# Kernel optimization log

Measured on AMD Instinct MI355X. Metric: run time of the kernel, lower is better.

The kernel has to match this reference:

```python
import jax, jax.numpy as jnp
import numpy as np

RPN_CLS_NEGATIVE = -1
RPN_CLS_NEUTRAL = 0
RPN_CLS_POSITIVE = 1

A = 261888  # anchors for 1024x1024 FPN, 3 per location
G = 256     # gt boxes


def _make_boxes(key, n, max_tl=900.0, min_sz=16.0, max_sz=124.0):
    k1, k2 = jax.random.split(key)
    tl = jax.random.uniform(k1, (n, 2), dtype=jnp.float32) * max_tl  # (y1, x1)
    wh = min_sz + jax.random.uniform(k2, (n, 2), dtype=jnp.float32) * (max_sz - min_sz)
    return jnp.concatenate([tl, tl + wh], axis=1)  # (y1, x1, y2, x2), all coords > 0


def setup_inputs() -> dict:
    key = jax.random.key(0)
    ka, kg, km, kc = jax.random.split(key, 4)
    anchors = _make_boxes(ka, A)
    gt_boxes = _make_boxes(kg, G)
    valid_anchors_mask = jax.random.uniform(km, (A,)) > 0.1
    gt_class_ids = jax.random.randint(kc, (G,), 1, 81, dtype=jnp.int32)
    bbox_std_dev = jnp.array([0.1, 0.1, 0.2, 0.2], dtype=jnp.float32)
    return {
        "anchors": anchors,
        "valid_anchors_mask": valid_anchors_mask,
        "gt_class_ids": gt_class_ids,
        "gt_boxes": gt_boxes,
        "bbox_std_dev": bbox_std_dev,
    }


def _compute_overlaps(b1, b2):
    """Pairwise IoU. b1: [N,4], b2: [M,4] -> [N,M]."""
    y1 = jnp.maximum(b1[:, None, 0], b2[None, :, 0])
    x1 = jnp.maximum(b1[:, None, 1], b2[None, :, 1])
    y2 = jnp.minimum(b1[:, None, 2], b2[None, :, 2])
    x2 = jnp.minimum(b1[:, None, 3], b2[None, :, 3])
    inter = jnp.maximum(y2 - y1, 0.0) * jnp.maximum(x2 - x1, 0.0)
    area1 = (b1[:, 2] - b1[:, 0]) * (b1[:, 3] - b1[:, 1])
    area2 = (b2[:, 2] - b2[:, 0]) * (b2[:, 3] - b2[:, 1])
    union = area1[:, None] + area2[None, :] - inter
    return inter / union


def reference(anchors, valid_anchors_mask, gt_class_ids, gt_boxes, bbox_std_dev):
    num_anchors = anchors.shape[0]
    is_crowd = gt_class_ids < 0  # [G]
    any_crowd = jnp.any(is_crowd)

    overlaps = _compute_overlaps(anchors, gt_boxes)  # [A, G]

    # crowd suppression (vectorized equivalent of the numpy crowd branch)
    crowd_iou_max = jnp.max(jnp.where(is_crowd[None, :], overlaps, 0.0), axis=1)
    no_crowd = jnp.where(any_crowd, crowd_iou_max < 0.001, True)

    # mask crowd columns out of the matching (numpy filters them from gt_boxes)
    ov = jnp.where(is_crowd[None, :], -1.0, overlaps)  # [A, G]
    anchor_iou_argmax = jnp.argmax(ov, axis=1)          # [A]
    anchor_iou_max = jnp.max(ov, axis=1)                # [A]

    # per-GT best anchor, restricted to valid anchors (numpy works on valid subset)
    ov_valid = jnp.where(valid_anchors_mask[:, None], ov, -1.0)
    gt_iou_argmax = jnp.argmax(ov_valid, axis=0)        # [G]
    pos_from_gt = jnp.zeros((num_anchors,), dtype=bool).at[gt_iou_argmax].max(~is_crowd)

    positive = pos_from_gt | (anchor_iou_max >= 0.7)
    negative = (anchor_iou_max < 0.3) & no_crowd & (~positive)

    rpn_match = jnp.where(positive, RPN_CLS_POSITIVE,
                          jnp.where(negative, RPN_CLS_NEGATIVE, RPN_CLS_NEUTRAL)).astype(jnp.int32)
    rpn_match = jnp.where(valid_anchors_mask, rpn_match, RPN_CLS_NEUTRAL)

    # deltas for positive anchors (faithful to source, incl. the `- -` -> `+` size bug)
    matched_gt = gt_boxes[anchor_iou_argmax]            # [A, 4]
    gt_size = matched_gt[:, 2:4] + matched_gt[:, 0:2]   # source: b[:,2:4] - -b[:,0:2]
    gt_centre = (matched_gt[:, 0:2] + matched_gt[:, 2:4]) * 0.5
    anc_size = anchors[:, 2:4] + anchors[:, 0:2]        # same bug
    anc_centre = (anchors[:, 0:2] + anchors[:, 2:4]) * 0.5
    deltas = jnp.concatenate([(gt_centre - anc_centre) / anc_size,
                              jnp.log(gt_size / anc_size)], axis=1)  # [A, 4]
    deltas = deltas / bbox_std_dev[None, :]  # RPN_BBOX_USE_STD_DEV = True

    pos_valid = positive & valid_anchors_mask
    rpn_bbox_all = jnp.where(pos_valid[:, None], deltas, 0.0).astype(jnp.float32)
    num_positives = jnp.sum(pos_valid).astype(jnp.int32)
    return rpn_match, rpn_bbox_all, num_positives
```

## Files before the change

kernel.cpp:

```cpp
#include <hip/hip_runtime.h>


#define GMAX 256
#define SHARDS 64
#define KBIAS 0xC0000001u
#define AIMASK 0x3FFFFu

__device__ __forceinline__ float4 compute_deltas(float4 ab, float4 gb,
                                                 const float* __restrict__ sd) {
    float sy_g = gb.z + gb.x;
    float sx_g = gb.w + gb.y;
    float sy_a = ab.z + ab.x;
    float sx_a = ab.w + ab.y;
    float4 d;
    d.x = (0.5f * (sy_g - sy_a) / sy_a) / sd[0];
    d.y = (0.5f * (sx_g - sx_a) / sx_a) / sd[1];
    d.z = logf(sy_g / sy_a) / sd[2];
    d.w = logf(sx_g / sx_a) / sd[3];
    return d;
}

__device__ __forceinline__ float iou_from(float4 ab, float a_area, float4 gb,
                                          float ga, float& inter) {
#pragma clang fp contract(off)
    float y1 = fmaxf(ab.x, gb.x);
    float x1 = fmaxf(ab.y, gb.y);
    float y2 = fminf(ab.z, gb.z);
    float x2 = fminf(ab.w, gb.w);
    inter = fmaxf(y2 - y1, 0.f) * fmaxf(x2 - x1, 0.f);
    return inter * __builtin_amdgcn_rcpf((a_area + ga) - inter);
}

__device__ __forceinline__ float iou_of(float4 ab, float a_area, float4 gb) {
    float y1 = fmaxf(ab.x, gb.x);
    float x1 = fmaxf(ab.y, gb.y);
    float y2 = fminf(ab.z, gb.z);
    float x2 = fminf(ab.w, gb.w);
    float inter = fmaxf(y2 - y1, 0.f) * fmaxf(x2 - x1, 0.f);
    float garea = (gb.z - gb.x) * (gb.w - gb.y);
    float uni = (a_area + garea) - inter;
    return inter * __builtin_amdgcn_rcpf(uni);
}

__global__ __launch_bounds__(256, 8) void rpn_main6(
    const float4* __restrict__ anchors,
    const int* __restrict__ valid,
    const int* __restrict__ cls,
    const float4* __restrict__ gt,
    const float* __restrict__ stdev,
    float* __restrict__ out,
    unsigned long long* __restrict__ gkeyS,
    int* __restrict__ pcount,
    int* __restrict__ fvmin,
    int A, int G)
{
    __shared__ float4 s_gt[GMAX];
    __shared__ float s_area[GMAX];
    __shared__ float s_crowdf[GMAX];
    __shared__ unsigned long long s_key[GMAX];
    __shared__ int s_anycrowd;
    __shared__ int s_cnt;
    __shared__ int s_fv;

    const int tid = threadIdx.x;
    if (tid == 0) { s_anycrowd = 0; s_cnt = 0; s_fv = 0x7FFFFFFF; }
    s_key[tid] = 0ULL;
    if (tid < G) {
        float4 b = gt[tid];
        s_gt[tid] = b;
        s_area[tid] = (b.z - b.x) * (b.w - b.y);
        int c = cls[tid];
        s_crowdf[tid] = (c < 0) ? 1.0f : 0.0f;
        if (c < 0) s_anycrowd = 1;
    }
    __syncthreads();
    const int any_crowd = s_anycrowd;

    const int a  = tid >> 2;
    const int h  = tid & 3;
    const int ai = blockIdx.x * 64 + a;
    const bool ir = (ai < A);
    float4 ab = ir ? anchors[ai] : make_float4(0.f, 0.f, 1.f, 1.f);
    const bool v = ir && (valid[ai] != 0);
    const float a_area = (ab.z - ab.x) * (ab.w - ab.y);

    const bool fast = (!any_crowd && G == GMAX);
    const int Gq = (G + 3) >> 2;

    float best = 0.0f;
    float cm = 0.0f;
    unsigned long long mm = 0ULL;
    int bg_final = 0;

    if (fast) {
        const float4* gp  = &s_gt[h];
        const float*  apb = &s_area[h];
        #pragma unroll
        for (int j = 0; j < 64; ++j) {
            float it;
            float iou = iou_from(ab, a_area, gp[j << 2], apb[j << 2], it);
            best = fmaxf(best, iou);
            if (it > 0.0f) mm |= (1ULL << j);
        }

        best = fmaxf(best, __shfl_xor(best, 1));
        best = fmaxf(best, __shfl_xor(best, 2));

        int bg_eq = 0x7FFFFFFF;
        if (best > 0.0f) {
            unsigned long long m = mm;
            while (m != 0ULL) {
                int j = __builtin_ctzll(m); m &= (m - 1ULL);
                int g = (j << 2) + h;
                float it;
                float iou = iou_from(ab, a_area, s_gt[g], s_area[g], it);
                if (iou == best) { bg_eq = g; break; }
            }
        }
        bg_eq = min(bg_eq, __shfl_xor(bg_eq, 1));
        bg_eq = min(bg_eq, __shfl_xor(bg_eq, 2));
        if (bg_eq != 0x7FFFFFFF) bg_final = bg_eq;
    } else {
        const int g0 = h * Gq;
        const int gn = max(0, min(G - g0, Gq));
        float bestg = -2.0f;
        int bg = min(g0, G - 1);
        for (int gg = 0; gg < gn; ++gg) {
            const int g = g0 + gg;
            float it;
            float iou = iou_from(ab, a_area, s_gt[g], s_area[g], it);
            float cf = s_crowdf[g];
            float eff = (cf != 0.0f) ? -1.0f : iou;
            if (eff > bestg) { bestg = eff; bg = g; }
            cm = fmaxf(cm, iou * cf);
            if (cf == 0.0f && iou > 0.0f) mm |= (1ULL << gg);
        }
        #pragma unroll
        for (int off = 1; off <= 2; off <<= 1) {
            float ob  = __shfl_xor(bestg, off);
            int   obg = __shfl_xor(bg, off);
            float ocm = __shfl_xor(cm, off);
            if (ob > bestg || (ob == bestg && obg < bg)) { bestg = ob; bg = obg; }
            cm = fmaxf(cm, ocm);
        }
        best = bestg;
        bg_final = bg;
    }

    bool no_crowd = any_crowd ? (cm < 0.001f) : true;
    bool pos = (best >= 0.7f);
    bool neg = (best < 0.3f) && no_crowd && !pos;
    bool posv = (h == 0) && pos && v;

    if (ir && h == 0) {
        out[ai] = v ? (pos ? 1.0f : (neg ? -1.0f : 0.0f)) : 0.0f;
        float4 d = make_float4(0.f, 0.f, 0.f, 0.f);
        if (pos && v) d = compute_deltas(ab, s_gt[bg_final], stdev);
        ((float4*)(out + A))[ai] = d;
    }

    if (v) {
        if (h == 0) atomicMin(&s_fv, ai);
        const unsigned long long lo =
            (((unsigned long long)((~(unsigned)ai) & AIMASK)) << 8) |
            (unsigned long long)((unsigned)bg_final & 0xFFu);
        unsigned long long m = mm;
        while (m != 0ULL) {
            int j = __builtin_ctzll(m); m &= (m - 1ULL);
            const int g = fast ? ((j << 2) + h) : (h * Gq + j);
            float it;
            float iou = iou_from(ab, a_area, s_gt[g], s_area[g], it);
            atomicMax(&s_key[g],
                (((unsigned long long)(__float_as_uint(iou) + KBIAS)) << 32) | lo);
        }
    }

    unsigned long long bal = __ballot((int)posv);
    if ((tid & 63) == 0) atomicAdd(&s_cnt, (int)__popcll(bal));
    __syncthreads();

    if (tid < G && s_key[tid] != 0ULL)
        atomicMax(&gkeyS[(size_t)tid * SHARDS + (blockIdx.x & (SHARDS - 1))],
                  s_key[tid]);
    if (tid == 0) { pcount[blockIdx.x] = s_cnt; fvmin[blockIdx.x] = s_fv; }
}

__global__ __launch_bounds__(1024) void rpn_finalize3(
    const float4* __restrict__ anchors,
    const int* __restrict__ cls,
    const float4* __restrict__ gt,
    const float* __restrict__ stdev,
    float* __restrict__ out,
    const unsigned long long* __restrict__ gkeyS,
    const int* __restrict__ pcount,
    const int* __restrict__ fvmin,
    int nb, int A, int G)
{
    __shared__ float4 s_gt[GMAX];
    __shared__ float s_area[GMAX];
    __shared__ float s_crowdf[GMAX];
    __shared__ int s_tot, s_fvr, s_flip;

    const int tid = threadIdx.x;
    if (tid == 0) { s_tot = 0; s_fvr = 0x7FFFFFFF; s_flip = 0; }
    if (tid < G) {
        float4 b = gt[tid];
        s_gt[tid] = b;
        s_area[tid] = (b.z - b.x) * (b.w - b.y);
        s_crowdf[tid] = (cls[tid] < 0) ? 1.0f : 0.0f;
    }
    __syncthreads();

    unsigned long long key = 0ULL;
    if (tid < G) {
        const unsigned long long* p = gkeyS + (size_t)tid * SHARDS;
        #pragma unroll
        for (int s = 0; s < SHARDS; s += 2) {
            ulonglong2 kv = *reinterpret_cast<const ulonglong2*>(p + s);
            unsigned long long k = (kv.x > kv.y) ? kv.x : kv.y;
            key = (k > key) ? k : key;
        }
    }
    if (tid >= 256) {
        int acc = 0, fv = 0x7FFFFFFF;
        for (int i = tid - 256; i < nb; i += 768) {
            acc += pcount[i];
            fv = min(fv, fvmin[i]);
        }
        #pragma unroll
        for (int off = 32; off >= 1; off >>= 1) {
            acc += __shfl_xor(acc, off);
            fv = min(fv, __shfl_xor(fv, off));
        }
        if ((tid & 63) == 0) { atomicAdd(&s_tot, acc); atomicMin(&s_fvr, fv); }
    }
    __syncthreads();

    bool flipped = false;
    if (tid < G && s_crowdf[tid] == 0.0f) {
        const bool has = ((unsigned)(key >> 32) >= (KBIAS + 1u));
        int w = -1, bg = -1;
        if (has) {
            w  = (int)((~((unsigned)key >> 8)) & AIMASK);
            bg = (int)((unsigned)key & 0xFFu);
        } else if (s_fvr != 0x7FFFFFFF) {
            w = s_fvr;
        }
        if (w >= 0) {
            float old = atomicExch(out + w, 1.0f);
            if (old != 1.0f) {
                if (bg < 0) {
                    float4 ab = anchors[w];
                    float aa = (ab.z - ab.x) * (ab.w - ab.y);
                    float bb = -2.0f; bg = 0;
                    for (int g = 0; g < G; ++g) {
                        float it;
                        float iou = iou_from(ab, aa, s_gt[g], s_area[g], it);
                        float eff = (s_crowdf[g] != 0.0f) ? -1.0f : iou;
                        if (eff > bb) { bb = eff; bg = g; }
                    }
                }
                ((float4*)(out + A))[w] = compute_deltas(anchors[w], s_gt[bg], stdev);
                flipped = true;
            }
        }
    }
    unsigned long long fb = __ballot((int)flipped);
    if (tid < 256 && (tid & 63) == 0) atomicAdd(&s_flip, (int)__popcll(fb));
    __syncthreads();
    if (tid == 0) out[(size_t)5 * A] = (float)(s_tot + s_flip);
}

__global__ __launch_bounds__(256) void rpn_fused(
    const float4* __restrict__ anchors, const int* __restrict__ valid,
    const int* __restrict__ cls, const float4* __restrict__ gt,
    const float* __restrict__ stdev, float* __restrict__ out,
    unsigned long long* __restrict__ gkey, unsigned* __restrict__ done,
    int* __restrict__ cnt, int A, int G)
{
    __shared__ float4 s_gt[GMAX];
    __shared__ float s_crowdf[GMAX];
    __shared__ unsigned long long s_key[GMAX];
    __shared__ int s_anycrowd; __shared__ int s_cnt; __shared__ int s_islast;

    const int tid = threadIdx.x;
    if (tid == 0) { s_anycrowd = 0; s_cnt = 0; }
    if (tid < G) {
        s_gt[tid] = gt[tid];
        int c = cls[tid];
        s_crowdf[tid] = (c < 0) ? 1.0f : 0.0f;
        if (c < 0) s_anycrowd = 1;
        s_key[tid] = 0ULL;
    }
    __syncthreads();
    const int any_crowd = s_anycrowd;
    const int ai = blockIdx.x * 256 + tid;
    const bool in_range = (ai < A);
    float4 ab = in_range ? anchors[ai] : make_float4(0.f, 0.f, 1.f, 1.f);
    const bool v = in_range && (valid[ai] != 0);
    const float a_area = (ab.z - ab.x) * (ab.w - ab.y);
    const unsigned lokey = ~(unsigned)ai;

    float best = any_crowd ? -2.0f : -1.0f;
    int bg = 0; float crowd_max = 0.0f;
    unsigned long long ovmask[4];
    #pragma unroll
    for (int w = 0; w < 4; ++w) {
        unsigned long long m = 0ULL;
        #pragma unroll 4
        for (int j = 0; j < 64; ++j) {
            int g = (w << 6) + j;
            if (g >= G) break;
            float iou = iou_of(ab, a_area, s_gt[g]);
            float cf = s_crowdf[g];
            float eff = (any_crowd && cf != 0.0f) ? -1.0f : iou;
            if (eff > best) { best = eff; bg = g; }
            if (any_crowd) crowd_max = fmaxf(crowd_max, iou * cf);
            if (v && (cf == 0.0f) && iou > 0.0f) m |= (1ULL << j);
        }
        ovmask[w] = m;
    }
    #pragma unroll
    for (int w = 0; w < 4; ++w) {
        unsigned long long m = ovmask[w];
        while (m != 0ULL) {
            int j = __builtin_ctzll(m); m &= (m - 1ULL);
            int g = (w << 6) + j;
            float iou = iou_of(ab, a_area, s_gt[g]);
            atomicMax(&s_key[g],
                (((unsigned long long)(__float_as_uint(iou) + 1u)) << 32) | lokey);
        }
    }
    bool no_crowd = any_crowd ? (crowd_max < 0.001f) : true;
    bool pos = (best >= 0.7f);
    bool neg = (best < 0.3f) && no_crowd && !pos;
    unsigned long long pv = __ballot((int)(in_range && pos && v));
    if ((tid & 63) == 0) atomicAdd(&s_cnt, (int)__popcll(pv));
    if (in_range) {
        out[ai] = v ? (pos ? 1.0f : (neg ? -1.0f : 0.0f)) : 0.0f;
        float4 d = make_float4(0.f, 0.f, 0.f, 0.f);
        if (pos && v) d = compute_deltas(ab, s_gt[bg], stdev);
        ((float4*)(out + A))[ai] = d;
    }
    __syncthreads();
    if (tid < G && s_key[tid] != 0ULL) atomicMax(&gkey[tid], s_key[tid]);
    if (tid == 0 && s_cnt > 0) atomicAdd(cnt, s_cnt);
    __threadfence();
    if (tid == 0) {
        unsigned prev = atomicAdd(done, 1u);
        s_islast = (prev == gridDim.x - 1);
        s_cnt = 0;
    }
    __syncthreads();
    if (!s_islast) return;
    __threadfence();
    if (tid < G && s_crowdf[tid] == 0.0f) {
        unsigned long long key = gkey[tid];
        int w;
        if (key != 0ULL) w = (int)(~(unsigned)(key & 0xFFFFFFFFull));
        else { w = 0; for (int i = 0; i < A; ++i) { if (valid[i] != 0) { w = i; break; } } }
        if (valid[w] != 0) {
            float old = atomicExch(out + w, 1.0f);
            if (old != 1.0f) {
                float4 ab2 = anchors[w];
                float a2 = (ab2.z - ab2.x) * (ab2.w - ab2.y);
                float b2 = -2.0f; int g2 = 0;
                for (int g = 0; g < G; ++g) {
                    float iou = iou_of(ab2, a2, s_gt[g]);
                    float eff = (s_crowdf[g] != 0.0f) ? -1.0f : iou;
                    if (eff > b2) { b2 = eff; g2 = g; }
                }
                ((float4*)(out + A))[w] = compute_deltas(ab2, s_gt[g2], stdev);
                atomicAdd(&s_cnt, 1);
            }
        }
    }
    __syncthreads();
    if (tid == 0) out[(size_t)5 * A] = (float)(*cnt + s_cnt);
}

extern "C" void kernel_launch(void* const* d_in, const int* in_sizes, int n_in,
                              void* d_out, int out_size, void* d_ws, size_t ws_size,
                              hipStream_t stream) {
    const float4* anchors = (const float4*)d_in[0];
    const int* valid      = (const int*)d_in[1];
    const int* cls        = (const int*)d_in[2];
    const float4* gtb     = (const float4*)d_in[3];
    const float* stdev    = (const float*)d_in[4];
    float* out            = (float*)d_out;

    const int A = in_sizes[0] / 4;
    const int G = in_sizes[2];
    const int nb4 = (A + 63) / 64;

    const size_t shard_bytes = (size_t)G * SHARDS * 8;
    const size_t pcnt_bytes  = (size_t)nb4 * 4;
    const size_t fv_bytes    = (size_t)nb4 * 4;
    const size_t needed = shard_bytes + pcnt_bytes + fv_bytes;

    if (ws_size >= needed && G <= GMAX && A <= (1 << 18)) {
        char* p = (char*)d_ws;
        unsigned long long* gkeyS = (unsigned long long*)p;          p += shard_bytes;
        int* pcount               = (int*)p;                         p += pcnt_bytes;
        int* fvmin                = (int*)p;

        rpn_main6<<<nb4, 256, 0, stream>>>(anchors, valid, cls, gtb, stdev, out,
                                           gkeyS, pcount, fvmin, A, G);
        rpn_finalize3<<<1, 1024, 0, stream>>>(anchors, cls, gtb, stdev, out,
                                              gkeyS, pcount, fvmin, nb4, A, G);
    } else {
        const int nb = (A + 255) / 256;
        unsigned long long* gkey = (unsigned long long*)d_ws;
        unsigned* done = (unsigned*)((char*)d_ws + 2048);
        int* cnt       = (int*)((char*)d_ws + 2052);
        hipMemsetAsync(d_ws, 0, 2056, stream);
        rpn_fused<<<nb, 256, 0, stream>>>(anchors, valid, cls, gtb, stdev, out,
                                          gkey, done, cnt, A, G);
    }
}
```

Baseline: 119.2 us.

## Bin gt boxes into a spatial grid per block to prune IoU candidates

Each block now buckets the gt boxes into an 8x8 grid of 128-pixel cells by their top-left corner, using a shared-memory prefix sum, and finds the largest gt height and width. Each anchor then computes IoU only against gt boxes in cells that could overlap it, instead of all 256, for both the best-match search and the per-gt max-key atomics. This cuts per-anchor IoU work, at the cost of extra setup and barriers in every block, data-dependent loop trip counts that cause divergence, and relying on gt coordinates being non-negative for correct binning.

```diff
diff --git a/kernel.cpp b/kernel.cpp
--- a/kernel.cpp
+++ b/kernel.cpp
@@ -42,7 +42,7 @@
     return inter * __builtin_amdgcn_rcpf(uni);
 }
 
-__global__ __launch_bounds__(256, 8) void rpn_main6(
+__global__ __launch_bounds__(256, 8) void rpn_main7(
     const float4* __restrict__ anchors,
     const int* __restrict__ valid,
     const int* __restrict__ cls,
@@ -58,13 +58,21 @@
     __shared__ float s_area[GMAX];
     __shared__ float s_crowdf[GMAX];
     __shared__ unsigned long long s_key[GMAX];
-    __shared__ int s_anycrowd;
-    __shared__ int s_cnt;
-    __shared__ int s_fv;
+    __shared__ unsigned short s_cellgt[GMAX];
+    __shared__ int s_cell[64];
+    __shared__ int s_cellcnt[64];
+    __shared__ int s_cur[64];
+    __shared__ int s_mhi, s_mwi;
+    __shared__ int s_anycrowd, s_cnt, s_fv;
 
     const int tid = threadIdx.x;
-    if (tid == 0) { s_anycrowd = 0; s_cnt = 0; s_fv = 0x7FFFFFFF; }
+    const float inv = 0.0078125f;
+    if (tid == 0) { s_anycrowd = 0; s_cnt = 0; s_fv = 0x7FFFFFFF; s_mhi = 0; s_mwi = 0; }
+    if (tid < 64) s_cellcnt[tid] = 0;
     s_key[tid] = 0ULL;
+
+    float gh = 0.f, gw = 0.f;
+    int mycell = 0;
     if (tid < G) {
         float4 b = gt[tid];
         s_gt[tid] = b;
@@ -72,9 +80,45 @@
         int c = cls[tid];
         s_crowdf[tid] = (c < 0) ? 1.0f : 0.0f;
         if (c < 0) s_anycrowd = 1;
-    }
-    __syncthreads();
+        gh = fmaxf(b.z - b.x, 0.f);
+        gw = fmaxf(b.w - b.y, 0.f);
+        int rr = max(0, min(7, (int)(b.x * inv)));
+        int cc = max(0, min(7, (int)(b.y * inv)));
+        mycell = (rr << 3) + cc;
+    }
+    #pragma unroll
+    for (int off = 32; off >= 1; off >>= 1) {
+        gh = fmaxf(gh, __shfl_xor(gh, off));
+        gw = fmaxf(gw, __shfl_xor(gw, off));
+    }
+    __syncthreads();
+    if (tid < G) atomicAdd(&s_cellcnt[mycell], 1);
+    if ((tid & 63) == 0) {
+        atomicMax(&s_mhi, __float_as_int(gh));
+        atomicMax(&s_mwi, __float_as_int(gw));
+    }
+    __syncthreads();
+    if (tid < 64) {
+        int v0 = s_cellcnt[tid];
+        int incl = v0;
+        #pragma unroll
+        for (int off = 1; off < 64; off <<= 1) {
+            int n = __shfl_up(incl, off);
+            if (tid >= off) incl += n;
+        }
+        s_cell[tid] = (incl - v0) | (v0 << 16);
+        s_cur[tid]  = incl - v0;
+    }
+    __syncthreads();
+    if (tid < G) {
+        int slot = atomicAdd(&s_cur[mycell], 1);
+        s_cellgt[slot] = (unsigned short)tid;
+    }
+    __syncthreads();
+
     const int any_crowd = s_anycrowd;
+    const float mh = __int_as_float(s_mhi);
+    const float mw = __int_as_float(s_mwi);
 
     const int a  = tid >> 2;
     const int h  = tid & 3;
@@ -84,45 +128,67 @@
     const bool v = ir && (valid[ai] != 0);
     const float a_area = (ab.z - ab.x) * (ab.w - ab.y);
 
-    const bool fast = (!any_crowd && G == GMAX);
-    const int Gq = (G + 3) >> 2;
-
     float best = 0.0f;
     float cm = 0.0f;
-    unsigned long long mm = 0ULL;
     int bg_final = 0;
 
-    if (fast) {
-        const float4* gp  = &s_gt[h];
-        const float*  apb = &s_area[h];
+    if (any_crowd == 0) {
+        float t0 = (ab.x - mh) * inv;
+        const int r0 = (t0 <= 0.f) ? 0 : min(7, (int)t0);
+        const int r1 = min(7, max(0, (int)(ab.z * inv)));
+        float u0 = (ab.y - mw) * inv;
+        const int c0 = (u0 <= 0.f) ? 0 : min(7, (int)u0);
+        const int c1 = min(7, max(0, (int)(ab.w * inv)));
+
+        float bb = 0.f; int bg = 0;
+        for (int r = r0; r <= r1; ++r) {
+            for (int c = c0; c <= c1; ++c) {
+                const unsigned sc = (unsigned)s_cell[(r << 3) + c];
+                const int start = (int)(sc & 0xFFFFu);
+                const int cnt   = (int)(sc >> 16);
+                for (int k = h; k < cnt; k += 4) {
+                    const int g = (int)s_cellgt[start + k];
+                    float it;
+                    float iou = iou_from(ab, a_area, s_gt[g], s_area[g], it);
+                    if (iou > bb) { bb = iou; bg = g; }
+                    else if (iou == bb && g < bg) bg = g;
+                }
+            }
+        }
         #pragma unroll
-        for (int j = 0; j < 64; ++j) {
-            float it;
-            float iou = iou_from(ab, a_area, gp[j << 2], apb[j << 2], it);
-            best = fmaxf(best, iou);
-            if (it > 0.0f) mm |= (1ULL << j);
-        }
-
-        best = fmaxf(best, __shfl_xor(best, 1));
-        best = fmaxf(best, __shfl_xor(best, 2));
-
-        int bg_eq = 0x7FFFFFFF;
-        if (best > 0.0f) {
-            unsigned long long m = mm;
-            while (m != 0ULL) {
-                int j = __builtin_ctzll(m); m &= (m - 1ULL);
-                int g = (j << 2) + h;
-                float it;
-                float iou = iou_from(ab, a_area, s_gt[g], s_area[g], it);
-                if (iou == best) { bg_eq = g; break; }
+        for (int off = 1; off <= 2; off <<= 1) {
+            float ob = __shfl_xor(bb, off);
+            int  obg = __shfl_xor(bg, off);
+            if (ob > bb || (ob == bb && obg < bg)) { bb = ob; bg = obg; }
+        }
+        best = bb; bg_final = bg;
+
+        if (v) {
+            if (h == 0) atomicMin(&s_fv, ai);
+            const unsigned long long lo =
+                (((unsigned long long)((~(unsigned)ai) & AIMASK)) << 8) |
+                (unsigned long long)((unsigned)bg_final & 0xFFu);
+            for (int r = r0; r <= r1; ++r) {
+                for (int c = c0; c <= c1; ++c) {
+                    const unsigned sc = (unsigned)s_cell[(r << 3) + c];
+                    const int start = (int)(sc & 0xFFFFu);
+                    const int cnt   = (int)(sc >> 16);
+                    for (int k = h; k < cnt; k += 4) {
+                        const int g = (int)s_cellgt[start + k];
+                        float it;
+                        float iou = iou_from(ab, a_area, s_gt[g], s_area[g], it);
+                        if (it > 0.f)
+                            atomicMax(&s_key[g],
+                                (((unsigned long long)(__float_as_uint(iou) + KBIAS)) << 32) | lo);
+                    }
+                }
             }
         }
-        bg_eq = min(bg_eq, __shfl_xor(bg_eq, 1));
-        bg_eq = min(bg_eq, __shfl_xor(bg_eq, 2));
-        if (bg_eq != 0x7FFFFFFF) bg_final = bg_eq;
     } else {
+        const int Gq = (G + 3) >> 2;
         const int g0 = h * Gq;
         const int gn = max(0, min(G - g0, Gq));
+        unsigned long long mm = 0ULL;
         float bestg = -2.0f;
         int bg = min(g0, G - 1);
         for (int gg = 0; gg < gn; ++gg) {
@@ -143,8 +209,23 @@
             if (ob > bestg || (ob == bestg && obg < bg)) { bestg = ob; bg = obg; }
             cm = fmaxf(cm, ocm);
         }
-        best = bestg;
-        bg_final = bg;
+        best = bestg; bg_final = bg;
+
+        if (v) {
+            if (h == 0) atomicMin(&s_fv, ai);
+            const unsigned long long lo =
+                (((unsigned long long)((~(unsigned)ai) & AIMASK)) << 8) |
+                (unsigned long long)((unsigned)bg_final & 0xFFu);
+            unsigned long long m = mm;
+            while (m != 0ULL) {
+                int j = __builtin_ctzll(m); m &= (m - 1ULL);
+                const int g = g0 + j;
+                float it;
+                float iou = iou_from(ab, a_area, s_gt[g], s_area[g], it);
+                atomicMax(&s_key[g],
+                    (((unsigned long long)(__float_as_uint(iou) + KBIAS)) << 32) | lo);
+            }
+        }
     }
 
     bool no_crowd = any_crowd ? (cm < 0.001f) : true;
@@ -157,22 +238,6 @@
         float4 d = make_float4(0.f, 0.f, 0.f, 0.f);
         if (pos && v) d = compute_deltas(ab, s_gt[bg_final], stdev);
         ((float4*)(out + A))[ai] = d;
-    }
-
-    if (v) {
-        if (h == 0) atomicMin(&s_fv, ai);
-        const unsigned long long lo =
-            (((unsigned long long)((~(unsigned)ai) & AIMASK)) << 8) |
-            (unsigned long long)((unsigned)bg_final & 0xFFu);
-        unsigned long long m = mm;
-        while (m != 0ULL) {
-            int j = __builtin_ctzll(m); m &= (m - 1ULL);
-            const int g = fast ? ((j << 2) + h) : (h * Gq + j);
-            float it;
-            float iou = iou_from(ab, a_area, s_gt[g], s_area[g], it);
-            atomicMax(&s_key[g],
-                (((unsigned long long)(__float_as_uint(iou) + KBIAS)) << 32) | lo);
-        }
     }
 
     unsigned long long bal = __ballot((int)posv);
@@ -404,7 +469,7 @@
         int* pcount               = (int*)p;                         p += pcnt_bytes;
         int* fvmin                = (int*)p;
 
-        rpn_main6<<<nb4, 256, 0, stream>>>(anchors, valid, cls, gtb, stdev, out,
+        rpn_main7<<<nb4, 256, 0, stream>>>(anchors, valid, cls, gtb, stdev, out,
                                            gkeyS, pcount, fvmin, A, G);
         rpn_finalize3<<<1, 1024, 0, stream>>>(anchors, cls, gtb, stdev, out,
                                               gkeyS, pcount, fvmin, nb4, A, G);
```

New measurement: 123.7 us. 3.8% more time.

## Process four anchors per thread to reuse each GT load across anchors

Applied to the files above, without the earlier changes.

Each block now covers 256 anchors instead of 64. In the fast path every thread evaluates four anchors against its quarter of the GT boxes, so each shared-memory GT load is reused four times. Per-thread results are picked out with select helpers for the output writes, and the first-valid-anchor tracking moves to a ballot-based atomicMin. The slow crowd path becomes one anchor per thread scanning all GTs. The cost is higher register pressure (launch bounds relaxed to 4 blocks) and four times fewer blocks, which feeds into the finalize kernel's per-block arrays.

```diff
diff --git a/kernel.cpp b/kernel.cpp
--- a/kernel.cpp
+++ b/kernel.cpp
@@ -42,7 +42,26 @@
     return inter * __builtin_amdgcn_rcpf(uni);
 }
 
-__global__ __launch_bounds__(256, 8) void rpn_main6(
+__device__ __forceinline__ float sel4f(float a0, float a1, float a2, float a3, int h) {
+    float lo = (h & 1) ? a1 : a0;
+    float hi = (h & 1) ? a3 : a2;
+    return (h & 2) ? hi : lo;
+}
+__device__ __forceinline__ int sel4i(int a0, int a1, int a2, int a3, int h) {
+    int lo = (h & 1) ? a1 : a0;
+    int hi = (h & 1) ? a3 : a2;
+    return (h & 2) ? hi : lo;
+}
+__device__ __forceinline__ float4 sel4f4(float4 a0, float4 a1, float4 a2, float4 a3, int h) {
+    float4 r;
+    r.x = sel4f(a0.x, a1.x, a2.x, a3.x, h);
+    r.y = sel4f(a0.y, a1.y, a2.y, a3.y, h);
+    r.z = sel4f(a0.z, a1.z, a2.z, a3.z, h);
+    r.w = sel4f(a0.w, a1.w, a2.w, a3.w, h);
+    return r;
+}
+
+__global__ __launch_bounds__(256, 4) void rpn_main8(
     const float4* __restrict__ anchors,
     const int* __restrict__ valid,
     const int* __restrict__ cls,
@@ -58,9 +77,7 @@
     __shared__ float s_area[GMAX];
     __shared__ float s_crowdf[GMAX];
     __shared__ unsigned long long s_key[GMAX];
-    __shared__ int s_anycrowd;
-    __shared__ int s_cnt;
-    __shared__ int s_fv;
+    __shared__ int s_anycrowd, s_cnt, s_fv;
 
     const int tid = threadIdx.x;
     if (tid == 0) { s_anycrowd = 0; s_cnt = 0; s_fv = 0x7FFFFFFF; }
@@ -76,107 +93,158 @@
     __syncthreads();
     const int any_crowd = s_anycrowd;
 
-    const int a  = tid >> 2;
-    const int h  = tid & 3;
-    const int ai = blockIdx.x * 64 + a;
-    const bool ir = (ai < A);
-    float4 ab = ir ? anchors[ai] : make_float4(0.f, 0.f, 1.f, 1.f);
-    const bool v = ir && (valid[ai] != 0);
-    const float a_area = (ab.z - ab.x) * (ab.w - ab.y);
-
-    const bool fast = (!any_crowd && G == GMAX);
-    const int Gq = (G + 3) >> 2;
-
-    float best = 0.0f;
-    float cm = 0.0f;
-    unsigned long long mm = 0ULL;
-    int bg_final = 0;
-
-    if (fast) {
+    const int q = tid >> 2;
+    const int h = tid & 3;
+    const int abase = blockIdx.x * 256 + (q << 2);
+    const int myai  = blockIdx.x * 256 + tid;
+    const bool myir = (myai < A);
+
+    bool posv = false, vmy = false;
+
+    if (!any_crowd && G == GMAX) {
+        float4 ab[4]; float aar[4]; int vld[4];
+        #pragma unroll
+        for (int k = 0; k < 4; ++k) {
+            const int ak = abase + k;
+            const bool irk = (ak < A);
+            ab[k]  = irk ? anchors[ak] : make_float4(0.f, 0.f, 1.f, 1.f);
+            vld[k] = irk ? valid[ak] : 0;
+            aar[k] = (ab[k].z - ab[k].x) * (ab[k].w - ab[k].y);
+        }
+
+        float best[4] = {0.f, 0.f, 0.f, 0.f};
+        unsigned long long msk[4] = {0ULL, 0ULL, 0ULL, 0ULL};
         const float4* gp  = &s_gt[h];
         const float*  apb = &s_area[h];
-        #pragma unroll
+        #pragma unroll 8
         for (int j = 0; j < 64; ++j) {
-            float it;
-            float iou = iou_from(ab, a_area, gp[j << 2], apb[j << 2], it);
-            best = fmaxf(best, iou);
-            if (it > 0.0f) mm |= (1ULL << j);
-        }
-
-        best = fmaxf(best, __shfl_xor(best, 1));
-        best = fmaxf(best, __shfl_xor(best, 2));
-
-        int bg_eq = 0x7FFFFFFF;
-        if (best > 0.0f) {
-            unsigned long long m = mm;
-            while (m != 0ULL) {
-                int j = __builtin_ctzll(m); m &= (m - 1ULL);
-                int g = (j << 2) + h;
+            float4 gb = gp[j << 2];
+            float  ga = apb[j << 2];
+            #pragma unroll
+            for (int k = 0; k < 4; ++k) {
                 float it;
-                float iou = iou_from(ab, a_area, s_gt[g], s_area[g], it);
-                if (iou == best) { bg_eq = g; break; }
-            }
-        }
-        bg_eq = min(bg_eq, __shfl_xor(bg_eq, 1));
-        bg_eq = min(bg_eq, __shfl_xor(bg_eq, 2));
-        if (bg_eq != 0x7FFFFFFF) bg_final = bg_eq;
+                float iou = iou_from(ab[k], aar[k], gb, ga, it);
+                best[k] = fmaxf(best[k], iou);
+                if (it > 0.f) msk[k] |= (1ULL << j);
+            }
+        }
+
+        float mb[4];
+        #pragma unroll
+        for (int k = 0; k < 4; ++k) {
+            float b = best[k];
+            b = fmaxf(b, __shfl_xor(b, 1));
+            b = fmaxf(b, __shfl_xor(b, 2));
+            mb[k] = b;
+        }
+        int bgm[4];
+        #pragma unroll
+        for (int k = 0; k < 4; ++k) {
+            int be = 0x7FFFFFFF;
+            if (mb[k] > 0.f) {
+                unsigned long long m = msk[k];
+                while (m != 0ULL) {
+                    int j = __builtin_ctzll(m); m &= (m - 1ULL);
+                    int g = (j << 2) + h;
+                    float it;
+                    float iou = iou_from(ab[k], aar[k], s_gt[g], s_area[g], it);
+                    if (iou == mb[k]) { be = g; break; }
+                }
+            }
+            be = min(be, __shfl_xor(be, 1));
+            be = min(be, __shfl_xor(be, 2));
+            bgm[k] = (be == 0x7FFFFFFF) ? 0 : be;
+        }
+
+        const float4 abm = sel4f4(ab[0], ab[1], ab[2], ab[3], h);
+        const float  mbm = sel4f(mb[0], mb[1], mb[2], mb[3], h);
+        const int    bgmy = sel4i(bgm[0], bgm[1], bgm[2], bgm[3], h);
+        const int    vm   = sel4i(vld[0], vld[1], vld[2], vld[3], h);
+        vmy = myir && (vm != 0);
+        bool pos = (mbm >= 0.7f);
+        bool neg = (mbm < 0.3f) && !pos;
+        posv = pos && vmy;
+        if (myir) {
+            out[myai] = vmy ? (pos ? 1.0f : (neg ? -1.0f : 0.0f)) : 0.0f;
+            float4 d = make_float4(0.f, 0.f, 0.f, 0.f);
+            if (pos && vmy) d = compute_deltas(abm, s_gt[bgmy], stdev);
+            ((float4*)(out + A))[myai] = d;
+        }
+
+        #pragma unroll
+        for (int k = 0; k < 4; ++k) {
+            if (vld[k]) {
+                const unsigned long long lo =
+                    (((unsigned long long)((~(unsigned)(abase + k)) & AIMASK)) << 8) |
+                    (unsigned long long)((unsigned)bgm[k] & 0xFFu);
+                unsigned long long m = msk[k];
+                while (m != 0ULL) {
+                    int j = __builtin_ctzll(m); m &= (m - 1ULL);
+                    int g = (j << 2) + h;
+                    float it;
+                    float iou = iou_from(ab[k], aar[k], s_gt[g], s_area[g], it);
+                    atomicMax(&s_key[g],
+                        (((unsigned long long)(__float_as_uint(iou) + KBIAS)) << 32) | lo);
+                }
+            }
+        }
     } else {
-        const int g0 = h * Gq;
-        const int gn = max(0, min(G - g0, Gq));
-        float bestg = -2.0f;
-        int bg = min(g0, G - 1);
-        for (int gg = 0; gg < gn; ++gg) {
-            const int g = g0 + gg;
-            float it;
-            float iou = iou_from(ab, a_area, s_gt[g], s_area[g], it);
-            float cf = s_crowdf[g];
-            float eff = (cf != 0.0f) ? -1.0f : iou;
-            if (eff > bestg) { bestg = eff; bg = g; }
-            cm = fmaxf(cm, iou * cf);
-            if (cf == 0.0f && iou > 0.0f) mm |= (1ULL << gg);
-        }
-        #pragma unroll
-        for (int off = 1; off <= 2; off <<= 1) {
-            float ob  = __shfl_xor(bestg, off);
-            int   obg = __shfl_xor(bg, off);
-            float ocm = __shfl_xor(cm, off);
-            if (ob > bestg || (ob == bestg && obg < bg)) { bestg = ob; bg = obg; }
-            cm = fmaxf(cm, ocm);
-        }
-        best = bestg;
-        bg_final = bg;
-    }
-
-    bool no_crowd = any_crowd ? (cm < 0.001f) : true;
-    bool pos = (best >= 0.7f);
-    bool neg = (best < 0.3f) && no_crowd && !pos;
-    bool posv = (h == 0) && pos && v;
-
-    if (ir && h == 0) {
-        out[ai] = v ? (pos ? 1.0f : (neg ? -1.0f : 0.0f)) : 0.0f;
-        float4 d = make_float4(0.f, 0.f, 0.f, 0.f);
-        if (pos && v) d = compute_deltas(ab, s_gt[bg_final], stdev);
-        ((float4*)(out + A))[ai] = d;
-    }
-
-    if (v) {
-        if (h == 0) atomicMin(&s_fv, ai);
-        const unsigned long long lo =
-            (((unsigned long long)((~(unsigned)ai) & AIMASK)) << 8) |
-            (unsigned long long)((unsigned)bg_final & 0xFFu);
-        unsigned long long m = mm;
-        while (m != 0ULL) {
-            int j = __builtin_ctzll(m); m &= (m - 1ULL);
-            const int g = fast ? ((j << 2) + h) : (h * Gq + j);
-            float it;
-            float iou = iou_from(ab, a_area, s_gt[g], s_area[g], it);
-            atomicMax(&s_key[g],
-                (((unsigned long long)(__float_as_uint(iou) + KBIAS)) << 32) | lo);
+        float4 ab2 = myir ? anchors[myai] : make_float4(0.f, 0.f, 1.f, 1.f);
+        int v2 = myir ? valid[myai] : 0;
+        float aa2 = (ab2.z - ab2.x) * (ab2.w - ab2.y);
+        float bb = -2.f; int bg = 0; float cmx = 0.f;
+        unsigned long long mk[4] = {0ULL, 0ULL, 0ULL, 0ULL};
+        #pragma unroll
+        for (int w = 0; w < 4; ++w) {
+            unsigned long long m = 0ULL;
+            for (int j = 0; j < 64; ++j) {
+                int g = (w << 6) + j;
+                if (g >= G) break;
+                float it;
+                float iou = iou_from(ab2, aa2, s_gt[g], s_area[g], it);
+                float cf = s_crowdf[g];
+                float eff = (cf != 0.f) ? -1.f : iou;
+                if (eff > bb) { bb = eff; bg = g; }
+                cmx = fmaxf(cmx, iou * cf);
+                if (cf == 0.f && it > 0.f) m |= (1ULL << j);
+            }
+            mk[w] = m;
+        }
+        bool no_crowd = (cmx < 0.001f);
+        vmy = myir && (v2 != 0);
+        bool pos = (bb >= 0.7f);
+        bool neg = (bb < 0.3f) && no_crowd && !pos;
+        posv = pos && vmy;
+        if (myir) {
+            out[myai] = vmy ? (pos ? 1.0f : (neg ? -1.0f : 0.0f)) : 0.0f;
+            float4 d = make_float4(0.f, 0.f, 0.f, 0.f);
+            if (pos && vmy) d = compute_deltas(ab2, s_gt[bg], stdev);
+            ((float4*)(out + A))[myai] = d;
+        }
+        if (vmy) {
+            const unsigned long long lo =
+                (((unsigned long long)((~(unsigned)myai) & AIMASK)) << 8) |
+                (unsigned long long)((unsigned)bg & 0xFFu);
+            #pragma unroll
+            for (int w = 0; w < 4; ++w) {
+                unsigned long long m = mk[w];
+                while (m != 0ULL) {
+                    int j = __builtin_ctzll(m); m &= (m - 1ULL);
+                    int g = (w << 6) + j;
+                    float it;
+                    float iou = iou_from(ab2, aa2, s_gt[g], s_area[g], it);
+                    atomicMax(&s_key[g],
+                        (((unsigned long long)(__float_as_uint(iou) + KBIAS)) << 32) | lo);
+                }
+            }
         }
     }
 
     unsigned long long bal = __ballot((int)posv);
     if ((tid & 63) == 0) atomicAdd(&s_cnt, (int)__popcll(bal));
+    unsigned long long vb = __ballot((int)vmy);
+    if ((tid & 63) == 0 && vb != 0ULL)
+        atomicMin(&s_fv, (int)(blockIdx.x * 256 + (tid & ~63) + (int)__builtin_ctzll(vb)));
     __syncthreads();
 
     if (tid < G && s_key[tid] != 0ULL)
@@ -391,7 +459,7 @@
 
     const int A = in_sizes[0] / 4;
     const int G = in_sizes[2];
-    const int nb4 = (A + 63) / 64;
+    const int nb4 = (A + 255) / 256;
 
     const size_t shard_bytes = (size_t)G * SHARDS * 8;
     const size_t pcnt_bytes  = (size_t)nb4 * 4;
@@ -404,7 +472,7 @@
         int* pcount               = (int*)p;                         p += pcnt_bytes;
         int* fvmin                = (int*)p;
 
-        rpn_main6<<<nb4, 256, 0, stream>>>(anchors, valid, cls, gtb, stdev, out,
+        rpn_main8<<<nb4, 256, 0, stream>>>(anchors, valid, cls, gtb, stdev, out,
                                            gkeyS, pcount, fvmin, A, G);
         rpn_finalize3<<<1, 1024, 0, stream>>>(anchors, cls, gtb, stdev, out,
                                               gkeyS, pcount, fvmin, nb4, A, G);
```

Measured after the change: 121.1 us. About the same (+1.7%).
